# Kernel optimization log

Hardware: AMD Instinct MI355X
Metric: run time of the kernel (lower is better)

## Reference

```python
import jax, jax.numpy as jnp
import numpy as np

B_, L_, D_, N_ = 4, 4096, 64, 16
DT = 0.1
EPS = 1e-6


def _complex_log(x):
    # log|x| (clamped) + i*pi for negative entries, matching torch impl
    real = jnp.log(jnp.maximum(jnp.abs(x), EPS))
    imag = jnp.where(x < 0, jnp.float32(np.pi), jnp.float32(0.0))
    return jax.lax.complex(real, imag)


def _clogaddexp(a, b):
    # stable complex log(exp(a)+exp(b)) using max of real parts
    m = jnp.maximum(a.real, b.real)
    return jnp.log(jnp.exp(a - m) + jnp.exp(b - m)) + m


def _clogcumsumexp(x, axis):
    return jax.lax.associative_scan(_clogaddexp, x, axis=axis)


def setup_inputs() -> dict:
    key = jax.random.key(0)
    ks = jax.random.split(key, 6)
    x = jax.random.normal(ks[0], (B_, L_, D_), jnp.float32)
    s = 1.0 / np.sqrt(D_)
    Wb = jax.random.uniform(ks[1], (N_, D_), jnp.float32, -s, s)
    bb = jax.random.uniform(ks[2], (N_,), jnp.float32, -s, s)
    Wc = jax.random.uniform(ks[3], (N_, D_), jnp.float32, -s, s)
    bc = jax.random.uniform(ks[4], (N_,), jnp.float32, -s, s)
    Wd = jax.random.uniform(ks[5], (1, D_), jnp.float32, -s, s)
    bd = jnp.zeros((1,), jnp.float32)
    # S4D-Real init: A_n = -(n+1), repeated over input_dim rows -> (D, N)
    A = jnp.tile(-(jnp.arange(N_, dtype=jnp.float32) + 1.0)[None, :], (D_, 1))
    return {"x": x, "A": A, "Wb": Wb, "bb": bb, "Wc": Wc, "bc": bc,
            "Wd": Wd, "bd": bd}


def reference(x, A, Wb, bb, Wc, bc, Wd, bd):
    # projections: (b,l,n)
    Bm = x @ Wb.T + bb
    Cm = x @ Wc.T + bc
    # delta network: softplus(linear(x)) + dt, broadcast to input_dim
    delta = jax.nn.softplus(x @ Wd.T + bd) + DT            # (b,l,1)
    dt = jnp.broadcast_to(delta, x.shape)                  # (b,l,d)
    # discretize
    tmp = A * dt[..., None]                                # (b,l,d,n)
    A_bar = jnp.exp(tmp)
    delta_B = jnp.einsum('bld,bln->bldn', dt, Bm)
    B_bar = (A_bar - 1.0) * delta_B / (tmp + EPS)
    term2 = B_bar * x[..., None]                           # (b,l,d,n)
    # parallel scan via complex log-cumsum-exp trick
    log_a = _complex_log(A_bar)
    log_b = _complex_log(term2)
    a_star = jnp.cumsum(log_a, axis=1)                     # (b,l,d,n) complex
    t = _clogcumsumexp(log_b - a_star, axis=1)
    scan = jnp.exp(a_star + t).real                        # (b,l,d,n)
    return jnp.sum(scan * Cm[:, :, None, :], axis=-1)      # (b,l,d)
```

## Files before the change

### kernel.cpp

```cpp
#include <hip/hip_runtime.h>

#define B_ 4
#define L_ 4096
#define D_ 64
#define N_ 16
#define CHUNK 32
#define NCHUNK (L_ / CHUNK)
#define TOTCHUNK (B_ * NCHUNK)
#define POS (B_ * L_)
#define POS_PER_BLK 8

constexpr float DT_  = 0.1f;
constexpr float EPS_ = 1e-6f;

__global__ __launch_bounds__(64) void proj_kernel(
    const float* __restrict__ x,  const float* __restrict__ A,
    const float* __restrict__ Wb, const float* __restrict__ bb,
    const float* __restrict__ Wc, const float* __restrict__ bc,
    const float* __restrict__ Wd, const float* __restrict__ bd,
    float* __restrict__ P, float* __restrict__ Cm)
{
    const int lane = threadIdx.x;
    const int o    = lane & 31;
    const int h2   = lane >> 5;
    __shared__ float xs[D_];

    float wreg[32];
    const float* Wrow = (o < 16) ? (Wb + o * D_) : (Wc + (o - 16) * D_);
    const float4* w4p = (const float4*)(Wrow + h2 * 32);
    #pragma unroll
    for (int j = 0; j < 8; j++) {
        float4 w4 = w4p[j];
        wreg[4*j+0] = w4.x; wreg[4*j+1] = w4.y;
        wreg[4*j+2] = w4.z; wreg[4*j+3] = w4.w;
    }
    const float wd   = Wd[lane];
    const float bd0  = bd[0];
    const float An   = A[lane & 15];
    const float bias = (o < 16) ? bb[o] : bc[o - 16];

    const int p0 = blockIdx.x * POS_PER_BLK;
    for (int p = p0; p < p0 + POS_PER_BLK; p++) {
        float xd = x[(size_t)p * D_ + lane];

        float r = xd * wd;
        #pragma unroll
        for (int m = 32; m >= 1; m >>= 1) r += __shfl_xor(r, m, 64);
        float z = r + bd0;
        float delta = fmaxf(z, 0.0f) + log1pf(expf(-fabsf(z))) + DT_;

        __syncthreads();
        xs[lane] = xd;
        __syncthreads();

        float acc = 0.0f;
        const float4* xs4 = (const float4*)(xs + h2 * 32);
        #pragma unroll
        for (int j = 0; j < 8; j++) {
            float4 v = xs4[j];
            acc += v.x * wreg[4*j+0] + v.y * wreg[4*j+1]
                 + v.z * wreg[4*j+2] + v.w * wreg[4*j+3];
        }
        acc += __shfl_xor(acc, 32, 64);

        if (lane < 16) {
            float Bm  = acc + bias;
            float tmp = An * delta;
            float a   = expf(tmp);
            float g   = (a - 1.0f) * delta * Bm / (tmp + EPS_);
            P[(size_t)p * 32 + lane]      = a;
            P[(size_t)p * 32 + 16 + lane] = g;
        } else if (lane < 32) {
            Cm[(size_t)p * 16 + (lane - 16)] = acc + bias;
        }
    }
}

__global__ __launch_bounds__(64) void scan_local(
    const float* __restrict__ x, const float* __restrict__ P,
    float* __restrict__ S, float* __restrict__ Cdec)
{
    const int gc    = blockIdx.x;
    const int batch = gc / NCHUNK;
    const int c     = gc % NCHUNK;
    const int lane  = threadIdx.x;
    const int base0 = batch * L_ + c * CHUNK;

    __shared__ float xs[CHUNK * D_];
    __shared__ float ag[CHUNK * 32];

    const float4* xg  = (const float4*)(x + (size_t)base0 * D_);
    float4*       xsv = (float4*)xs;
    #pragma unroll
    for (int i = 0; i < 8; i++) xsv[i * 64 + lane] = xg[i * 64 + lane];
    const float4* pg  = (const float4*)(P + (size_t)base0 * 32);
    float4*       agv = (float4*)ag;
    #pragma unroll
    for (int i = 0; i < 4; i++) agv[i * 64 + lane] = pg[i * 64 + lane];
    __syncthreads();

    float h[N_], cum[N_];
    #pragma unroll
    for (int n = 0; n < N_; n++) { h[n] = 0.0f; cum[n] = 1.0f; }

    for (int s = 0; s < CHUNK; s++) {
        float xd = xs[s * D_ + lane];
        const float4* row = (const float4*)(ag + s * 32);
        #pragma unroll
        for (int q = 0; q < 4; q++) {
            float4 a4 = row[q];
            float4 g4 = row[4 + q];
            h[4*q+0] = a4.x * h[4*q+0] + g4.x * xd;  cum[4*q+0] *= a4.x;
            h[4*q+1] = a4.y * h[4*q+1] + g4.y * xd;  cum[4*q+1] *= a4.y;
            h[4*q+2] = a4.z * h[4*q+2] + g4.z * xd;  cum[4*q+2] *= a4.z;
            h[4*q+3] = a4.w * h[4*q+3] + g4.w * xd;  cum[4*q+3] *= a4.w;
        }
    }

    #pragma unroll
    for (int n = 0; n < N_; n++)
        S[(size_t)(gc * N_ + n) * D_ + lane] = h[n];
    if (lane == 0) {
        #pragma unroll
        for (int n = 0; n < N_; n++) Cdec[gc * N_ + n] = cum[n];
    }
}

__global__ __launch_bounds__(64) void combine(
    float* __restrict__ S, const float* __restrict__ Cdec)
{
    const int b = blockIdx.x >> 4;
    const int n = blockIdx.x & 15;
    const int d = threadIdx.x;

    float run = 0.0f;
    #pragma unroll 4
    for (int c = 0; c < NCHUNK; c++) {
        const int    gc  = b * NCHUNK + c;
        const size_t idx = (size_t)(gc * N_ + n) * D_ + d;
        float s = S[idx];
        float a = Cdec[gc * N_ + n];
        S[idx] = run;
        run = a * run + s;
    }
}

__global__ __launch_bounds__(64) void scan_out(
    const float* __restrict__ x, const float* __restrict__ P,
    const float* __restrict__ Cmat, const float* __restrict__ S,
    float* __restrict__ out)
{
    const int gc    = blockIdx.x;
    const int batch = gc / NCHUNK;
    const int c     = gc % NCHUNK;
    const int lane  = threadIdx.x;
    const int base0 = batch * L_ + c * CHUNK;

    __shared__ float xs[CHUNK * D_];
    __shared__ float ag[CHUNK * 32];
    __shared__ float cm[CHUNK * N_];

    const float4* xg  = (const float4*)(x + (size_t)base0 * D_);
    float4*       xsv = (float4*)xs;
    #pragma unroll
    for (int i = 0; i < 8; i++) xsv[i * 64 + lane] = xg[i * 64 + lane];
    const float4* pg  = (const float4*)(P + (size_t)base0 * 32);
    float4*       agv = (float4*)ag;
    #pragma unroll
    for (int i = 0; i < 4; i++) agv[i * 64 + lane] = pg[i * 64 + lane];
    const float4* cg  = (const float4*)(Cmat + (size_t)base0 * 16);
    float4*       cmv = (float4*)cm;
    #pragma unroll
    for (int i = 0; i < 2; i++) cmv[i * 64 + lane] = cg[i * 64 + lane];
    __syncthreads();

    float h[N_];
    #pragma unroll
    for (int n = 0; n < N_; n++)
        h[n] = S[(size_t)(gc * N_ + n) * D_ + lane];

    for (int s = 0; s < CHUNK; s++) {
        float xd = xs[s * D_ + lane];
        const float4* row = (const float4*)(ag + s * 32);
        const float4* crw = (const float4*)(cm + s * 16);
        float acc = 0.0f;
        #pragma unroll
        for (int q = 0; q < 4; q++) {
            float4 a4 = row[q];
            float4 g4 = row[4 + q];
            float4 c4 = crw[q];
            h[4*q+0] = a4.x * h[4*q+0] + g4.x * xd;  acc += c4.x * h[4*q+0];
            h[4*q+1] = a4.y * h[4*q+1] + g4.y * xd;  acc += c4.y * h[4*q+1];
            h[4*q+2] = a4.z * h[4*q+2] + g4.z * xd;  acc += c4.z * h[4*q+2];
            h[4*q+3] = a4.w * h[4*q+3] + g4.w * xd;  acc += c4.w * h[4*q+3];
        }
        out[(size_t)(base0 + s) * D_ + lane] = acc;
    }
}

extern "C" void kernel_launch(void* const* d_in, const int* in_sizes, int n_in,
                              void* d_out, int out_size, void* d_ws, size_t ws_size,
                              hipStream_t stream)
{
    const float* x  = (const float*)d_in[0];
    const float* A  = (const float*)d_in[1];
    const float* Wb = (const float*)d_in[2];
    const float* bb = (const float*)d_in[3];
    const float* Wc = (const float*)d_in[4];
    const float* bc = (const float*)d_in[5];
    const float* Wd = (const float*)d_in[6];
    const float* bd = (const float*)d_in[7];
    float* out = (float*)d_out;

    float* P    = (float*)d_ws;
    float* Cm   = P  + (size_t)B_ * L_ * 32;
    float* S    = Cm + (size_t)B_ * L_ * 16;
    float* Cdec = S  + (size_t)TOTCHUNK * N_ * D_;

    proj_kernel<<<POS / POS_PER_BLK, 64, 0, stream>>>(x, A, Wb, bb, Wc, bc, Wd, bd, P, Cm);
    scan_local<<<TOTCHUNK, 64, 0, stream>>>(x, P, S, Cdec);
    combine<<<B_ * N_, 64, 0, stream>>>(S, Cdec);
    scan_out<<<TOTCHUNK, 64, 0, stream>>>(x, P, Cm, S, out);
}
```

Measured before the change: 115.9 us.

## Halve scan chunk size, batch projection loads, prefetch in combine

Scan chunk length drops from 32 to 16. This doubles the number of chunk blocks in the local and output scans (more parallelism, shorter serial loops) but also doubles the length of the serial combine pass over chunks. The combine kernel now software-prefetches the next four chunk states and decays to hide global-load latency in its serial recurrence. The projection kernel loads all eight positions' inputs into shared memory at once, batches the delta reductions, and removes the per-position barriers.

Result: faster. 110.0 us (-5.1%).

```diff
diff --git a/kernel.cpp b/kernel.cpp
--- a/kernel.cpp
+++ b/kernel.cpp
@@ -4,7 +4,7 @@
 #define L_ 4096
 #define D_ 64
 #define N_ 16
-#define CHUNK 32
+#define CHUNK 16
 #define NCHUNK (L_ / CHUNK)
 #define TOTCHUNK (B_ * NCHUNK)
 #define POS (B_ * L_)
@@ -23,7 +23,7 @@
     const int lane = threadIdx.x;
     const int o    = lane & 31;
     const int h2   = lane >> 5;
-    __shared__ float xs[D_];
+    __shared__ float xs[POS_PER_BLK * D_];
 
     float wreg[32];
     const float* Wrow = (o < 16) ? (Wb + o * D_) : (Wc + (o - 16) * D_);
@@ -40,21 +40,32 @@
     const float bias = (o < 16) ? bb[o] : bc[o - 16];
 
     const int p0 = blockIdx.x * POS_PER_BLK;
-    for (int p = p0; p < p0 + POS_PER_BLK; p++) {
-        float xd = x[(size_t)p * D_ + lane];
-
-        float r = xd * wd;
-        #pragma unroll
-        for (int m = 32; m >= 1; m >>= 1) r += __shfl_xor(r, m, 64);
-        float z = r + bd0;
-        float delta = fmaxf(z, 0.0f) + log1pf(expf(-fabsf(z))) + DT_;
-
-        __syncthreads();
-        xs[lane] = xd;
-        __syncthreads();
-
+
+    const float4* xg  = (const float4*)(x + (size_t)p0 * D_);
+    float4*       xsv = (float4*)xs;
+    xsv[lane]      = xg[lane];
+    xsv[64 + lane] = xg[64 + lane];
+    __syncthreads();
+
+    float r[POS_PER_BLK];
+    #pragma unroll
+    for (int p = 0; p < POS_PER_BLK; p++) r[p] = xs[p * D_ + lane] * wd;
+    #pragma unroll
+    for (int m = 32; m >= 1; m >>= 1) {
+        #pragma unroll
+        for (int p = 0; p < POS_PER_BLK; p++) r[p] += __shfl_xor(r[p], m, 64);
+    }
+    float delta[POS_PER_BLK];
+    #pragma unroll
+    for (int p = 0; p < POS_PER_BLK; p++) {
+        float z = r[p] + bd0;
+        delta[p] = fmaxf(z, 0.0f) + log1pf(expf(-fabsf(z))) + DT_;
+    }
+
+    #pragma unroll
+    for (int p = 0; p < POS_PER_BLK; p++) {
         float acc = 0.0f;
-        const float4* xs4 = (const float4*)(xs + h2 * 32);
+        const float4* xs4 = (const float4*)(xs + p * D_ + h2 * 32);
         #pragma unroll
         for (int j = 0; j < 8; j++) {
             float4 v = xs4[j];
@@ -62,16 +73,16 @@
                  + v.z * wreg[4*j+2] + v.w * wreg[4*j+3];
         }
         acc += __shfl_xor(acc, 32, 64);
-
+        const int pp = p0 + p;
         if (lane < 16) {
             float Bm  = acc + bias;
-            float tmp = An * delta;
+            float tmp = An * delta[p];
             float a   = expf(tmp);
-            float g   = (a - 1.0f) * delta * Bm / (tmp + EPS_);
-            P[(size_t)p * 32 + lane]      = a;
-            P[(size_t)p * 32 + 16 + lane] = g;
+            float g   = (a - 1.0f) * delta[p] * Bm / (tmp + EPS_);
+            P[(size_t)pp * 32 + lane]      = a;
+            P[(size_t)pp * 32 + 16 + lane] = g;
         } else if (lane < 32) {
-            Cm[(size_t)p * 16 + (lane - 16)] = acc + bias;
+            Cm[(size_t)pp * 16 + (lane - 16)] = acc + bias;
         }
     }
 }
@@ -92,11 +103,11 @@
     const float4* xg  = (const float4*)(x + (size_t)base0 * D_);
     float4*       xsv = (float4*)xs;
     #pragma unroll
-    for (int i = 0; i < 8; i++) xsv[i * 64 + lane] = xg[i * 64 + lane];
+    for (int i = 0; i < 4; i++) xsv[i * 64 + lane] = xg[i * 64 + lane];
     const float4* pg  = (const float4*)(P + (size_t)base0 * 32);
     float4*       agv = (float4*)ag;
     #pragma unroll
-    for (int i = 0; i < 4; i++) agv[i * 64 + lane] = pg[i * 64 + lane];
+    for (int i = 0; i < 2; i++) agv[i * 64 + lane] = pg[i * 64 + lane];
     __syncthreads();
 
     float h[N_], cum[N_];
@@ -132,16 +143,30 @@
     const int b = blockIdx.x >> 4;
     const int n = blockIdx.x & 15;
     const int d = threadIdx.x;
+    const int cb = b * NCHUNK;
 
     float run = 0.0f;
-    #pragma unroll 4
-    for (int c = 0; c < NCHUNK; c++) {
-        const int    gc  = b * NCHUNK + c;
-        const size_t idx = (size_t)(gc * N_ + n) * D_ + d;
-        float s = S[idx];
-        float a = Cdec[gc * N_ + n];
-        S[idx] = run;
-        run = a * run + s;
+    float sbuf[4], abuf[4];
+    #pragma unroll
+    for (int j = 0; j < 4; j++) {
+        sbuf[j] = S[(size_t)((cb + j) * N_ + n) * D_ + d];
+        abuf[j] = Cdec[(cb + j) * N_ + n];
+    }
+    for (int c = 0; c < NCHUNK; c += 4) {
+        const int cn = (c + 4 < NCHUNK) ? c + 4 : c;
+        float t[4], u[4];
+        #pragma unroll
+        for (int j = 0; j < 4; j++) {
+            t[j] = S[(size_t)((cb + cn + j) * N_ + n) * D_ + d];
+            u[j] = Cdec[(cb + cn + j) * N_ + n];
+        }
+        #pragma unroll
+        for (int j = 0; j < 4; j++) {
+            S[(size_t)((cb + c + j) * N_ + n) * D_ + d] = run;
+            run = abuf[j] * run + sbuf[j];
+        }
+        #pragma unroll
+        for (int j = 0; j < 4; j++) { sbuf[j] = t[j]; abuf[j] = u[j]; }
     }
 }
 
@@ -163,15 +188,14 @@
     const float4* xg  = (const float4*)(x + (size_t)base0 * D_);
     float4*       xsv = (float4*)xs;
     #pragma unroll
-    for (int i = 0; i < 8; i++) xsv[i * 64 + lane] = xg[i * 64 + lane];
+    for (int i = 0; i < 4; i++) xsv[i * 64 + lane] = xg[i * 64 + lane];
     const float4* pg  = (const float4*)(P + (size_t)base0 * 32);
     float4*       agv = (float4*)ag;
     #pragma unroll
-    for (int i = 0; i < 4; i++) agv[i * 64 + lane] = pg[i * 64 + lane];
+    for (int i = 0; i < 2; i++) agv[i * 64 + lane] = pg[i * 64 + lane];
     const float4* cg  = (const float4*)(Cmat + (size_t)base0 * 16);
     float4*       cmv = (float4*)cm;
-    #pragma unroll
-    for (int i = 0; i < 2; i++) cmv[i * 64 + lane] = cg[i * 64 + lane];
+    cmv[lane] = cg[lane];
     __syncthreads();
 
     float h[N_];
```
